# Optimization experiments

Hardware: AMD Instinct MI355X
Metric: run time of the kernel (lower is better)

Reference implementation:

```python
import jax, jax.numpy as jnp
import numpy as np

B, N, NODE_DIM = 32, 512, 2
D, H, L, FF = 512, 8, 3, 2048
DK = D // H  # key/val dim per head = 64
EPS = 1e-5


def batch_norm(h, gamma, beta):
    # BatchNorm1d in training mode over flattened (batch*graph) dim, biased var
    flat = h.reshape(-1, h.shape[-1])
    mu = flat.mean(axis=0)
    var = flat.var(axis=0)
    out = (flat - mu) * jax.lax.rsqrt(var + EPS) * gamma + beta
    return out.reshape(h.shape)


def mha(h, Wq, Wk, Wv, Wo):
    # h: [B,N,D]; Wq/Wk/Wv: [H,D,DK]; Wo: [H,DK,D]
    Q = jnp.einsum('bnd,hdk->hbnk', h, Wq)
    K = jnp.einsum('bnd,hdk->hbnk', h, Wk)
    V = jnp.einsum('bnd,hdk->hbnk', h, Wv)
    scores = jnp.einsum('hbqk,hbnk->hbqn', Q, K) / jnp.sqrt(jnp.float32(DK))
    attn = jax.nn.softmax(scores, axis=-1)
    heads = jnp.einsum('hbqn,hbnk->hbqk', attn, V)
    return jnp.einsum('hbqk,hkd->bqd', heads, Wo)


def setup_inputs() -> dict:
    key = jax.random.key(0)
    ks = jax.random.split(key, 16)
    u = lambda k, shape, fan: jax.random.uniform(k, shape, jnp.float32, -1.0, 1.0) / np.sqrt(fan)
    return {
        'x': jax.random.normal(ks[0], (B, N, NODE_DIM), jnp.float32),
        'We': u(ks[1], (D, NODE_DIM), NODE_DIM),
        'be': u(ks[2], (D,), NODE_DIM),
        'Wq': u(ks[3], (L, H, D, DK), DK),
        'Wk': u(ks[4], (L, H, D, DK), DK),
        'Wv': u(ks[5], (L, H, D, DK), DK),
        'Wo': u(ks[6], (L, H, DK, D), D),
        'g1': jnp.ones((L, D), jnp.float32),
        'b1': jnp.zeros((L, D), jnp.float32),
        'W1': u(ks[7], (L, FF, D), D),
        'bb1': u(ks[8], (L, FF), D),
        'W2': u(ks[9], (L, D, FF), FF),
        'bb2': u(ks[10], (L, D), FF),
        'g2': jnp.ones((L, D), jnp.float32),
        'b2': jnp.zeros((L, D), jnp.float32),
    }


def reference(x, We, be, Wq, Wk, Wv, Wo, g1, b1, W1, bb1, W2, bb2, g2, b2):
    # init embed: Linear(node_dim -> D)
    h = jnp.einsum('bnc,dc->bnd', x, We) + be
    for i in range(L):
        h = batch_norm(h + mha(h, Wq[i], Wk[i], Wv[i], Wo[i]), g1[i], b1[i])
        ff = jax.nn.relu(jnp.einsum('bnd,fd->bnf', h, W1[i]) + bb1[i])
        ff = jnp.einsum('bnf,df->bnd', ff, W2[i]) + bb2[i]
        h = batch_norm(h + ff, g2[i], b2[i])
    return h, h.mean(axis=1)
```

## Files before the change

### kernel.cpp

```cpp
#include <hip/hip_runtime.h>
#include <hip/hip_bf16.h>

#define Bx 32
#define Nx 512
#define Dx 512
#define Hx 8
#define DKx 64
#define FFx 2048
#define TOK (Bx * Nx)
#define EPSx 1e-5f

typedef float  f32x4  __attribute__((ext_vector_type(4)));
typedef _Float16 hfrag8 __attribute__((ext_vector_type(8)));
typedef _Float16 h4     __attribute__((ext_vector_type(4)));
typedef _Float16 h2     __attribute__((ext_vector_type(2)));

struct hf2 { _Float16 hi, lo; };
__device__ __forceinline__ hf2 split2h(float v) {
    _Float16 h = (_Float16)v;
    hf2 r; r.hi = h; r.lo = (_Float16)(v - (float)h);
    return r;
}

__device__ __forceinline__ void gl16(const void* g, void* l) {
    __builtin_amdgcn_global_load_lds(
        (const __attribute__((address_space(1))) unsigned int*)g,
        (__attribute__((address_space(3))) unsigned int*)l, 16, 0, 0);
}

__device__ __forceinline__ int swzoff(int row, int q) {
    int p = row >> 1;
    int sl = ((row & 1) << 2) | q;
    int s = sl ^ (p & 7);
    return p * 128 + s * 16;
}

__device__ __forceinline__ float ldsel(const void* p32, const void* p16, size_t i, int f32) {
    return f32 ? ((const float*)p32)[i]
               : __bfloat162float(((const __hip_bfloat16*)p16)[i]);
}

__global__ void detect_kernel(const void* __restrict__ x, int* __restrict__ flag)
{
    if (threadIdx.x == 0 && blockIdx.x == 0) {
        const unsigned short* u = (const unsigned short*)x;
        int hits = 0;
        for (int i = 0; i < 256; ++i) {
            int e = (u[i] >> 7) & 0xFF;
            if (e >= 0x86) ++hits;
        }
        *flag = (hits > 8) ? 1 : 0;
    }
}

__global__ __launch_bounds__(256) void cvt_kernel(
    const void* __restrict__ W, _Float16* __restrict__ o, const int* __restrict__ dtp)
{
    const int f32 = *dtp;
    size_t idx = (size_t)blockIdx.x * 256 + threadIdx.x;
    o[idx] = (_Float16)ldsel(W, W, idx, f32);
}

__global__ __launch_bounds__(256) void transpose_cvt_kernel(
    const void* __restrict__ W, _Float16* __restrict__ o,
    int R, int C, const int* __restrict__ dtp)
{
    const int f32 = *dtp;
    __shared__ float tile[64][65];
    const size_t mbase = (size_t)blockIdx.z * R * C;
    const int c0 = blockIdx.x * 64, r0 = blockIdx.y * 64;
    const int tc = threadIdx.x & 63, tg = threadIdx.x >> 6;
    #pragma unroll
    for (int i = 0; i < 16; ++i) {
        int r = tg * 16 + i;
        tile[r][tc] = ldsel(W, W, mbase + (size_t)(r0 + r) * C + c0 + tc, f32);
    }
    __syncthreads();
    #pragma unroll
    for (int i = 0; i < 16; ++i) {
        int cc = tg * 16 + i;
        o[mbase + (size_t)(c0 + cc) * R + r0 + tc] = (_Float16)tile[tc][cc];
    }
}

__global__ __launch_bounds__(256) void embed_kernel(
    const void* __restrict__ x, const void* __restrict__ We,
    const void* __restrict__ be, _Float16* __restrict__ hh, _Float16* __restrict__ hl,
    const int* __restrict__ dtp)
{
    const int f32 = *dtp;
    size_t idx = (size_t)blockIdx.x * 256 + threadIdx.x;
    int d = idx & (Dx - 1);
    size_t t = idx >> 9;
    float v = ldsel(x, x, t * 2, f32)     * ldsel(We, We, d * 2, f32) +
              ldsel(x, x, t * 2 + 1, f32) * ldsel(We, We, d * 2 + 1, f32) +
              ldsel(be, be, d, f32);
    hf2 s = split2h(v);
    hh[idx] = s.hi; hl[idx] = s.lo;
}

template <int EPI, int OHF, int STATS>
__global__ __launch_bounds__(256, 3) void gemm3(
    const _Float16* __restrict__ Ahg, const _Float16* __restrict__ Bg,
    const void* __restrict__ bias32, const void* __restrict__ bias16,
    const _Float16* __restrict__ residH, const _Float16* __restrict__ residL,
    void* __restrict__ outp, float* __restrict__ part,
    int M, int N, int K, const int* __restrict__ dtp)
{
    const int f32 = *dtp;
    __shared__ __align__(16) unsigned char lds[3][2 * 8192];

    const int tid = threadIdx.x;
    const int gx = gridDim.x;
    const int nwg = gx * gridDim.y;
    int flat = blockIdx.y * gx + blockIdx.x;
    flat = (flat & 7) * (nwg >> 3) + (flat >> 3);
    const int bm = (flat / gx) * 128;
    const int bn = (flat % gx) * 128;

    const int lane = tid & 63, wv = tid >> 6;
    const int quad = lane >> 4, lrow = lane & 15;
    const int wm = (wv & 1) * 64, wn = (wv >> 1) * 64;

    f32x4 acc[4][4] = {};

    const int s2 = (lane & 7) ^ (lane >> 3);
    const int rl = 2 * (lane >> 3) + (s2 >> 2);
    const int cl = (s2 & 3) * 8;

    const bool doStage = (wv < 2);
    const _Float16* wsrc = (wv == 0) ? Ahg : Bg;
    const int wrb = (wv == 0) ? bm : bn;

    auto stage = [&](int buf, int k0) {
        if (doStage) {
            const _Float16* s = wsrc + (size_t)(wrb + rl) * K + k0 + cl;
            #pragma unroll
            for (int ch = 0; ch < 8; ++ch)
                gl16(s + (size_t)(ch * 16) * K, &lds[buf][wv * 8192 + ch * 1024]);
        }
    };

    int offA[4], offB[4];
    #pragma unroll
    for (int mt = 0; mt < 4; ++mt) offA[mt] = swzoff(wm + mt * 16 + lrow, quad);
    #pragma unroll
    for (int nt = 0; nt < 4; ++nt) offB[nt] = 8192 + swzoff(wn + nt * 16 + lrow, quad);

    const int NT = K >> 5;
    stage(0, 0);
    stage(1, 32);

    for (int i = 0; i < NT; ++i) {
        if (i + 1 < NT) asm volatile("s_waitcnt vmcnt(8)" ::: "memory");
        else            asm volatile("s_waitcnt vmcnt(0)" ::: "memory");
        __builtin_amdgcn_sched_barrier(0);
        __builtin_amdgcn_s_barrier();
        __builtin_amdgcn_sched_barrier(0);

        if (i + 2 < NT) stage((i + 2) % 3, (i + 2) << 5);

        const unsigned char* bp = lds[i % 3];
        hfrag8 ah[4];
        #pragma unroll
        for (int mt = 0; mt < 4; ++mt)
            ah[mt] = *(const hfrag8*)(bp + offA[mt]);
        #pragma unroll
        for (int nt = 0; nt < 4; ++nt) {
            hfrag8 b = *(const hfrag8*)(bp + offB[nt]);
            #pragma unroll
            for (int mt = 0; mt < 4; ++mt)
                acc[mt][nt] = __builtin_amdgcn_mfma_f32_16x16x32_f16(ah[mt], b, acc[mt][nt], 0, 0, 0);
        }

        __builtin_amdgcn_sched_barrier(0);
        asm volatile("s_waitcnt lgkmcnt(0)" ::: "memory");
        __builtin_amdgcn_sched_barrier(0);
    }

    #pragma unroll
    for (int nt = 0; nt < 4; ++nt) {
        const int n = bn + wn + nt * 16 + lrow;
        float cs = 0.f, cq = 0.f;
        #pragma unroll
        for (int mt = 0; mt < 4; ++mt)
            #pragma unroll
            for (int reg = 0; reg < 4; ++reg) {
                int m = bm + wm + mt * 16 + quad * 4 + reg;
                float v = acc[mt][nt][reg];
                if constexpr (EPI == 1) { v += ldsel(bias32, bias16, n, f32); v = fmaxf(v, 0.f); }
                if constexpr (EPI == 2) {
                    if (bias32) v += ldsel(bias32, bias16, n, f32);
                    size_t ridx = (size_t)m * N + n;
                    v += (float)residH[ridx] + (float)residL[ridx];
                }
                size_t oidx = (size_t)m * N + n;
                if constexpr (OHF == 1) ((_Float16*)outp)[oidx] = (_Float16)v;
                else if constexpr (OHF == 2) {
                    hf2 s = split2h(v);
                    h2 pk; pk[0] = s.hi; pk[1] = s.lo;
                    ((h2*)outp)[oidx] = pk;
                }
                else ((float*)outp)[oidx] = v;
                if constexpr (STATS) { cs += v; cq += v * v; }
            }
        if constexpr (STATS) {
            cs += __shfl_xor(cs, 16); cs += __shfl_xor(cs, 32);
            cq += __shfl_xor(cq, 16); cq += __shfl_xor(cq, 32);
            if (quad == 0) {
                float* pb = part + (size_t)(bm >> 7) * 1024;
                atomicAdd(&pb[n], cs);
                atomicAdd(&pb[512 + n], cq);
            }
        }
    }
}

__global__ __launch_bounds__(256, 3) void qkv_mfma(
    const _Float16* __restrict__ Ahg,
    const _Float16* __restrict__ QT, const _Float16* __restrict__ KT,
    const _Float16* __restrict__ VT,
    _Float16* __restrict__ Qhg, _Float16* __restrict__ Qlg,
    _Float16* __restrict__ Khg, _Float16* __restrict__ Vo, int M, int K)
{
    __shared__ __align__(16) unsigned char lds[3][2 * 8192];

    const int tid = threadIdx.x;
    const int gx = gridDim.x;
    const int nwg = gx * gridDim.y;
    int flat = blockIdx.y * gx + blockIdx.x;
    flat = (flat & 7) * (nwg >> 3) + (flat >> 3);
    const int bm = (flat / gx) * 128;
    const int bn = (flat % gx) * 128;

    const int sel = bn >> 9;
    const int nloc = bn & 511;
    const _Float16* Bg = ((sel == 0) ? QT : (sel == 1) ? KT : VT) + (size_t)nloc * K;

    const int lane = tid & 63, wv = tid >> 6;
    const int quad = lane >> 4, lrow = lane & 15;
    const int wm = (wv & 1) * 64, wn = (wv >> 1) * 64;

    f32x4 acc[4][4] = {};

    const int s2 = (lane & 7) ^ (lane >> 3);
    const int rl = 2 * (lane >> 3) + (s2 >> 2);
    const int cl = (s2 & 3) * 8;

    const bool doStage = (wv < 2);
    const _Float16* wsrc = (wv == 0) ? Ahg : Bg;
    const int wrb = (wv == 0) ? bm : 0;

    auto stage = [&](int buf, int k0) {
        if (doStage) {
            const _Float16* s = wsrc + (size_t)(wrb + rl) * K + k0 + cl;
            #pragma unroll
            for (int ch = 0; ch < 8; ++ch)
                gl16(s + (size_t)(ch * 16) * K, &lds[buf][wv * 8192 + ch * 1024]);
        }
    };

    int offA[4], offB[4];
    #pragma unroll
    for (int mt = 0; mt < 4; ++mt) offA[mt] = swzoff(wm + mt * 16 + lrow, quad);
    #pragma unroll
    for (int nt = 0; nt < 4; ++nt) offB[nt] = 8192 + swzoff(wn + nt * 16 + lrow, quad);

    const int NT = K >> 5;
    stage(0, 0);
    stage(1, 32);

    for (int i = 0; i < NT; ++i) {
        if (i + 1 < NT) asm volatile("s_waitcnt vmcnt(8)" ::: "memory");
        else            asm volatile("s_waitcnt vmcnt(0)" ::: "memory");
        __builtin_amdgcn_sched_barrier(0);
        __builtin_amdgcn_s_barrier();
        __builtin_amdgcn_sched_barrier(0);

        if (i + 2 < NT) stage((i + 2) % 3, (i + 2) << 5);

        const unsigned char* bp = lds[i % 3];
        hfrag8 ah[4];
        #pragma unroll
        for (int mt = 0; mt < 4; ++mt)
            ah[mt] = *(const hfrag8*)(bp + offA[mt]);
        #pragma unroll
        for (int nt = 0; nt < 4; ++nt) {
            hfrag8 b = *(const hfrag8*)(bp + offB[nt]);
            #pragma unroll
            for (int mt = 0; mt < 4; ++mt)
                acc[mt][nt] = __builtin_amdgcn_mfma_f32_16x16x32_f16(ah[mt], b, acc[mt][nt], 0, 0, 0);
        }

        __builtin_amdgcn_sched_barrier(0);
        asm volatile("s_waitcnt lgkmcnt(0)" ::: "memory");
        __builtin_amdgcn_sched_barrier(0);
    }

    const int nb = M >> 9;
    #pragma unroll
    for (int mt = 0; mt < 4; ++mt)
        #pragma unroll
        for (int nt = 0; nt < 4; ++nt) {
            const int ncol = nloc + wn + nt * 16 + lrow;
            const int head = ncol >> 6, dk = ncol & 63;
            const int m0 = bm + wm + mt * 16 + quad * 4;
            const int b_ = m0 >> 9, q = m0 & 511;
            if (sel == 2) {
                h4 v;
                #pragma unroll
                for (int reg = 0; reg < 4; ++reg) v[reg] = (_Float16)acc[mt][nt][reg];
                *(h4*)&Vo[(((size_t)head * nb + b_) * DKx + dk) * Nx + q] = v;
            } else if (sel == 1) {
                #pragma unroll
                for (int reg = 0; reg < 4; ++reg) {
                    size_t oidx = (((size_t)head * nb + b_) * Nx + (q + reg)) * DKx + dk;
                    Khg[oidx] = (_Float16)acc[mt][nt][reg];
                }
            } else {
                #pragma unroll
                for (int reg = 0; reg < 4; ++reg) {
                    hf2 s = split2h(acc[mt][nt][reg]);
                    size_t oidx = (((size_t)head * nb + b_) * Nx + (q + reg)) * DKx + dk;
                    Qhg[oidx] = s.hi;
                    Qlg[oidx] = s.lo;
                }
            }
        }
}

__global__ __launch_bounds__(256, 4) void attn_kernel(
    const _Float16* __restrict__ Qhg, const _Float16* __restrict__ Qlg,
    const _Float16* __restrict__ Khg, const _Float16* __restrict__ Vtg,
    _Float16* __restrict__ heads)
{
    __shared__ __align__(16) _Float16  Kh[64][72];
    __shared__ __align__(16) _Float16  Vt[64][72];
    __shared__ __align__(16) _Float16  Sp[64][72];
    __shared__ float ml[64], ll[64], al[64];

    const int tid = threadIdx.x;
    const int q0 = blockIdx.x * 64;
    const int hb = blockIdx.y;
    const size_t base = (size_t)hb * (Nx * DKx);
    const int lane = tid & 63, wv = tid >> 6;
    const int quad = lane >> 4, lrow = lane & 15;
    const int wm = (wv & 1) * 32, wn = (wv >> 1) * 32;
    const int sr = tid >> 2, sc = (tid & 3) * 16;

    {
        size_t off = base + (size_t)(q0 + sr) * DKx + sc;
        *(hfrag8*)&Kh[sr][sc]     = *(const hfrag8*)(Qhg + off);
        *(hfrag8*)&Kh[sr][sc + 8] = *(const hfrag8*)(Qhg + off + 8);
        *(hfrag8*)&Sp[sr][sc]     = *(const hfrag8*)(Qlg + off);
        *(hfrag8*)&Sp[sr][sc + 8] = *(const hfrag8*)(Qlg + off + 8);
    }
    if (tid < 64) { ml[tid] = -INFINITY; ll[tid] = 0.f; }
    __syncthreads();

    hfrag8 qh[2][2], qlo[2][2];
    #pragma unroll
    for (int mt = 0; mt < 2; ++mt)
        #pragma unroll
        for (int ks = 0; ks < 2; ++ks) {
            qh[mt][ks]  = *(const hfrag8*)&Kh[wm + mt * 16 + lrow][ks * 32 + quad * 8];
            qlo[mt][ks] = *(const hfrag8*)&Sp[wm + mt * 16 + lrow][ks * 32 + quad * 8];
        }
    __syncthreads();

    hfrag8 pkh[2], pv[2];
    auto loadKV = [&](int n0) {
        size_t off = base + (size_t)(n0 + sr) * DKx + sc;
        pkh[0] = *(const hfrag8*)(Khg + off);
        pkh[1] = *(const hfrag8*)(Khg + off + 8);
        const _Float16* vp = Vtg + base + (size_t)sr * Nx + n0 + sc;
        pv[0] = *(const hfrag8*)vp;
        pv[1] = *(const hfrag8*)(vp + 8);
    };
    auto storeKV = [&]() {
        *(hfrag8*)&Kh[sr][sc]     = pkh[0];
        *(hfrag8*)&Kh[sr][sc + 8] = pkh[1];
        *(hfrag8*)&Vt[sr][sc]     = pv[0];
        *(hfrag8*)&Vt[sr][sc + 8] = pv[1];
    };

    f32x4 accO[2][2] = {};

    loadKV(0); storeKV();
    __syncthreads();

    for (int n0 = 0; n0 < Nx; n0 += 64) {
        const bool more = (n0 + 64 < Nx);
        if (more) loadKV(n0 + 64);

        f32x4 accS[2][2] = {};
        __builtin_amdgcn_s_setprio(1);
        #pragma unroll
        for (int ks = 0; ks < 2; ++ks) {
            hfrag8 bh[2];
            #pragma unroll
            for (int nt = 0; nt < 2; ++nt)
                bh[nt] = *(const hfrag8*)&Kh[wn + nt * 16 + lrow][ks * 32 + quad * 8];
            #pragma unroll
            for (int mt = 0; mt < 2; ++mt)
                #pragma unroll
                for (int nt = 0; nt < 2; ++nt) {
                    accS[mt][nt] = __builtin_amdgcn_mfma_f32_16x16x32_f16(qh[mt][ks],  bh[nt], accS[mt][nt], 0, 0, 0);
                    accS[mt][nt] = __builtin_amdgcn_mfma_f32_16x16x32_f16(qlo[mt][ks], bh[nt], accS[mt][nt], 0, 0, 0);
                }
        }
        __builtin_amdgcn_s_setprio(0);
        #pragma unroll
        for (int mt = 0; mt < 2; ++mt)
            #pragma unroll
            for (int nt = 0; nt < 2; ++nt)
                #pragma unroll
                for (int reg = 0; reg < 4; ++reg)
                    Sp[wm + mt * 16 + quad * 4 + reg][wn + nt * 16 + lrow] =
                        (_Float16)(accS[mt][nt][reg] * 0.125f);
        __syncthreads();

        {
            hfrag8 s0 = *(const hfrag8*)&Sp[sr][sc];
            hfrag8 s1 = *(const hfrag8*)&Sp[sr][sc + 8];
            float rmax = -INFINITY;
            #pragma unroll
            for (int j = 0; j < 8; ++j) {
                rmax = fmaxf(rmax, (float)s0[j]);
                rmax = fmaxf(rmax, (float)s1[j]);
            }
            rmax = fmaxf(rmax, __shfl_xor(rmax, 1));
            rmax = fmaxf(rmax, __shfl_xor(rmax, 2));
            float mold = ml[sr];
            float mnew = fmaxf(mold, rmax);
            float sum = 0.f;
            hfrag8 p0, p1;
            #pragma unroll
            for (int j = 0; j < 8; ++j) {
                float pa = __expf((float)s0[j] - mnew);
                float pb = __expf((float)s1[j] - mnew);
                sum += pa + pb;
                p0[j] = (_Float16)pa;
                p1[j] = (_Float16)pb;
            }
            sum += __shfl_xor(sum, 1);
            sum += __shfl_xor(sum, 2);
            *(hfrag8*)&Sp[sr][sc]     = p0;
            *(hfrag8*)&Sp[sr][sc + 8] = p1;
            if ((tid & 3) == 0) {
                float alpha = __expf(mold - mnew);
                ml[sr] = mnew;
                ll[sr] = ll[sr] * alpha + sum;
                al[sr] = alpha;
            }
        }
        __syncthreads();

        #pragma unroll
        for (int mt = 0; mt < 2; ++mt) {
            float a0 = al[wm + mt * 16 + quad * 4 + 0];
            float a1 = al[wm + mt * 16 + quad * 4 + 1];
            float a2 = al[wm + mt * 16 + quad * 4 + 2];
            float a3 = al[wm + mt * 16 + quad * 4 + 3];
            #pragma unroll
            for (int nt = 0; nt < 2; ++nt) {
                accO[mt][nt][0] *= a0; accO[mt][nt][1] *= a1;
                accO[mt][nt][2] *= a2; accO[mt][nt][3] *= a3;
            }
        }
        __builtin_amdgcn_s_setprio(1);
        #pragma unroll
        for (int ks = 0; ks < 2; ++ks) {
            hfrag8 ap[2], bv[2];
            #pragma unroll
            for (int mt = 0; mt < 2; ++mt)
                ap[mt] = *(const hfrag8*)&Sp[wm + mt * 16 + lrow][ks * 32 + quad * 8];
            #pragma unroll
            for (int nt = 0; nt < 2; ++nt)
                bv[nt] = *(const hfrag8*)&Vt[wn + nt * 16 + lrow][ks * 32 + quad * 8];
            #pragma unroll
            for (int mt = 0; mt < 2; ++mt)
                #pragma unroll
                for (int nt = 0; nt < 2; ++nt)
                    accO[mt][nt] = __builtin_amdgcn_mfma_f32_16x16x32_f16(ap[mt], bv[nt], accO[mt][nt], 0, 0, 0);
        }
        __builtin_amdgcn_s_setprio(0);

        if (more) {
            __syncthreads();
            storeKV();
            __syncthreads();
        }
    }

    const int h_ = hb >> 5, b_ = hb & 31;
    #pragma unroll
    for (int mt = 0; mt < 2; ++mt)
        #pragma unroll
        for (int reg = 0; reg < 4; ++reg) {
            int qrow = wm + mt * 16 + quad * 4 + reg;
            float invl = 1.f / ll[qrow];
            size_t tok = (size_t)b_ * Nx + (q0 + qrow);
            #pragma unroll
            for (int nt = 0; nt < 2; ++nt) {
                int dk = wn + nt * 16 + lrow;
                heads[tok * Dx + h_ * DKx + dk] = (_Float16)(accO[mt][nt][reg] * invl);
            }
        }
}

__global__ __launch_bounds__(256) void bn_final(
    const float* __restrict__ part, float* __restrict__ stats)
{
    int c = blockIdx.x * 256 + threadIdx.x;
    float s = 0.f;
    for (int rt = 0; rt < 128; ++rt) s += part[(size_t)rt * 1024 + c];
    stats[c] = s;
}

__global__ __launch_bounds__(256) void bn_norm(
    const h2* __restrict__ tpk, const float* __restrict__ stats,
    const void* __restrict__ g32, const void* __restrict__ g16,
    const void* __restrict__ b32, const void* __restrict__ b16,
    _Float16* __restrict__ hh, _Float16* __restrict__ hl,
    float* __restrict__ out32, const int* __restrict__ dtp)
{
    const int f32 = *dtp;
    size_t idx = (size_t)blockIdx.x * 256 + threadIdx.x;
    int c = idx & (Dx - 1);
    const float invM = 1.f / (float)TOK;
    float mu = stats[c] * invM;
    float var = stats[Dx + c] * invM - mu * mu;
    h2 tv = tpk[idx];
    float t = (float)tv[0] + (float)tv[1];
    float v = (t - mu) * rsqrtf(var + EPSx) * ldsel(g32, g16, c, f32) + ldsel(b32, b16, c, f32);
    hf2 s = split2h(v);
    hh[idx] = s.hi; hl[idx] = s.lo;
    if (out32) out32[idx] = v;
}

__global__ __launch_bounds__(256) void out_mean_part(
    const _Float16* __restrict__ hh, const _Float16* __restrict__ hl, float* __restrict__ part)
{
    int b = blockIdx.x;
    int g = blockIdx.y;
    int d = threadIdx.x;
    float s0 = 0.f, s1 = 0.f;
    for (int n = g * 64; n < g * 64 + 64; ++n) {
        size_t idx = ((size_t)b * Nx + n) * Dx;
        s0 += (float)hh[idx + d]       + (float)hl[idx + d];
        s1 += (float)hh[idx + d + 256] + (float)hl[idx + d + 256];
    }
    part[((size_t)b * 8 + g) * Dx + d]       = s0;
    part[((size_t)b * 8 + g) * Dx + d + 256] = s1;
}

__global__ __launch_bounds__(256) void out_mean_final(
    const float* __restrict__ part, float* __restrict__ out2)
{
    size_t o = (size_t)blockIdx.x * 256 + threadIdx.x;
    int b = (int)(o >> 9), d = (int)(o & 511);
    float s = 0.f;
    #pragma unroll
    for (int g = 0; g < 8; ++g) s += part[((size_t)b * 8 + g) * Dx + d];
    out2[o] = s * (1.f / (float)Nx);
}

extern "C" void kernel_launch(void* const* d_in, const int* in_sizes, int n_in,
                              void* d_out, int out_size, void* d_ws, size_t ws_size,
                              hipStream_t stream)
{
    const void* x   = d_in[0];
    const void* We  = d_in[1];
    const void* be  = d_in[2];
    const void* Wq  = d_in[3];
    const void* Wk  = d_in[4];
    const void* Wv  = d_in[5];
    const void* Wo  = d_in[6];
    const void* g1  = d_in[7];
    const void* b1  = d_in[8];
    const void* W1  = d_in[9];
    const void* bb1 = d_in[10];
    const void* W2  = d_in[11];
    const void* bb2 = d_in[12];
    const void* g2  = d_in[13];
    const void* b2  = d_in[14];

    const size_t szHD = (size_t)TOK * Dx;
    const size_t QKN  = (size_t)Hx * Bx * Nx * DKx;
    const size_t szQT = (size_t)3 * Hx * DKx * Dx;
    const size_t szW1 = (size_t)3 * FFx * Dx;
    const size_t szWqkvL = (size_t)Hx * Dx * DKx;

    h2* tpk        = (h2*)d_ws;
    float* stats   = (float*)(tpk + szHD);
    int*   dtp     = (int*)(stats + 2 * Dx);
    _Float16* hh   = (_Float16*)(stats + 2 * Dx + 64);
    _Float16* hl   = hh + szHD;
    _Float16* region = hl + szHD;

    _Float16* heads = region;
    _Float16* Qhg   = heads + szHD;
    _Float16* Qlg   = Qhg + QKN;
    _Float16* Khg   = Qlg + QKN;
    _Float16* Vtg   = Khg + QKN;
    _Float16* ffbuf = region;

    _Float16* WqT = Vtg + QKN;
    _Float16* WkT = WqT + szQT;
    _Float16* WvT = WkT + szQT;
    _Float16* WoT = WvT + szQT;
    _Float16* W1c = WoT + szQT;
    _Float16* W2c = W1c + szW1;
    float*    part = (float*)(W2c + szW1);

    auto p32 = [](const void* p, size_t e) { return (const void*)((const float*)p + e); };
    auto p16 = [](const void* p, size_t e) { return (const void*)((const __hip_bfloat16*)p + e); };

    detect_kernel<<<1, 64, 0, stream>>>(x, dtp);

    transpose_cvt_kernel<<<dim3(1, 8, 24), 256, 0, stream>>>(Wq, WqT, Dx, DKx, dtp);
    transpose_cvt_kernel<<<dim3(1, 8, 24), 256, 0, stream>>>(Wk, WkT, Dx, DKx, dtp);
    transpose_cvt_kernel<<<dim3(1, 8, 24), 256, 0, stream>>>(Wv, WvT, Dx, DKx, dtp);
    transpose_cvt_kernel<<<dim3(8, 8, 3), 256, 0, stream>>>(Wo, WoT, Dx, Dx, dtp);
    cvt_kernel<<<szW1 / 256, 256, 0, stream>>>(W1, W1c, dtp);
    cvt_kernel<<<szW1 / 256, 256, 0, stream>>>(W2, W2c, dtp);

    embed_kernel<<<TOK * Dx / 256, 256, 0, stream>>>(x, We, be, hh, hl, dtp);

    const dim3 gQKV(12, TOK / 128);
    const dim3 gWo(Dx / 128, TOK / 128);
    const dim3 gAttn(Nx / 64, Hx * Bx);
    const dim3 gFF1(FFx / 128, TOK / 128);
    const dim3 gFF2(Dx / 128, TOK / 128);
    const size_t partBytes = 128 * 1024 * sizeof(float);
    for (int l = 0; l < 3; ++l) {
        const size_t eQ = (size_t)l * szWqkvL;
        const size_t e1 = (size_t)l * FFx * Dx;
        const size_t eD = (size_t)l * Dx, eF = (size_t)l * FFx;
        const bool last = (l == 2);

        qkv_mfma<<<gQKV, 256, 0, stream>>>(
            hh, WqT + eQ, WkT + eQ, WvT + eQ,
            Qhg, Qlg, Khg, Vtg, TOK, Dx);
        attn_kernel<<<gAttn, 256, 0, stream>>>(Qhg, Qlg, Khg, Vtg, heads);

        hipMemsetAsync(part, 0, partBytes, stream);
        gemm3<2, 2, 1><<<gWo, 256, 0, stream>>>(
            heads, WoT + eQ,
            nullptr, nullptr, hh, hl, tpk, part, TOK, Dx, Dx, dtp);
        bn_final<<<4, 256, 0, stream>>>(part, stats);
        bn_norm<<<TOK * Dx / 256, 256, 0, stream>>>(
            tpk, stats, p32(g1, eD), p16(g1, eD), p32(b1, eD), p16(b1, eD),
            hh, hl, nullptr, dtp);

        gemm3<1, 1, 0><<<gFF1, 256, 0, stream>>>(
            hh, W1c + e1,
            p32(bb1, eF), p16(bb1, eF), nullptr, nullptr, ffbuf, nullptr,
            TOK, FFx, Dx, dtp);
        hipMemsetAsync(part, 0, partBytes, stream);
        gemm3<2, 2, 1><<<gFF2, 256, 0, stream>>>(
            ffbuf, W2c + e1,
            p32(bb2, eD), p16(bb2, eD), hh, hl, tpk, part, TOK, Dx, FFx, dtp);
        bn_final<<<4, 256, 0, stream>>>(part, stats);
        bn_norm<<<TOK * Dx / 256, 256, 0, stream>>>(
            tpk, stats, p32(g2, eD), p16(g2, eD), p32(b2, eD), p16(b2, eD),
            hh, hl, last ? (float*)d_out : nullptr, dtp);
    }

    out_mean_part<<<dim3(Bx, 8), 256, 0, stream>>>(hh, hl, part);
    out_mean_final<<<Bx * Dx / 256, 256, 0, stream>>>(part, (float*)d_out + (size_t)TOK * Dx);
}
```

Measured before the change: 1.200 ms.

## Widen GEMM output tiles to 128x256 with three staging waves

Both the generic GEMM and the fused QKV GEMM move from 128x128 to 128x256 output tiles. Each wave now holds a 64x128 accumulator, and a third wave stages the second half of the B tile into a larger LDS buffer. The aim is better operand reuse per LDS load and fewer A-tile reloads from global memory. In exchange, register pressure roughly doubles, occupancy bounds drop from 3 to 2 workgroups, and the grids shrink by half. The batch-norm partial buffer is enlarged and indexed by 64-row blocks, and bn_final now sums 256 partial rows.

```diff
diff --git a/kernel.cpp b/kernel.cpp
--- a/kernel.cpp
+++ b/kernel.cpp
@@ -100,7 +100,7 @@
 }
 
 template <int EPI, int OHF, int STATS>
-__global__ __launch_bounds__(256, 3) void gemm3(
+__global__ __launch_bounds__(256, 2) void gemm3(
     const _Float16* __restrict__ Ahg, const _Float16* __restrict__ Bg,
     const void* __restrict__ bias32, const void* __restrict__ bias16,
     const _Float16* __restrict__ residH, const _Float16* __restrict__ residL,
@@ -108,7 +108,7 @@
     int M, int N, int K, const int* __restrict__ dtp)
 {
     const int f32 = *dtp;
-    __shared__ __align__(16) unsigned char lds[3][2 * 8192];
+    __shared__ __align__(16) unsigned char lds[3][24576];
 
     const int tid = threadIdx.x;
     const int gx = gridDim.x;
@@ -116,40 +116,44 @@
     int flat = blockIdx.y * gx + blockIdx.x;
     flat = (flat & 7) * (nwg >> 3) + (flat >> 3);
     const int bm = (flat / gx) * 128;
-    const int bn = (flat % gx) * 128;
+    const int bn = (flat % gx) * 256;
 
     const int lane = tid & 63, wv = tid >> 6;
     const int quad = lane >> 4, lrow = lane & 15;
-    const int wm = (wv & 1) * 64, wn = (wv >> 1) * 64;
-
-    f32x4 acc[4][4] = {};
+    const int wm = (wv & 1) * 64, wn = (wv >> 1) * 128;
+
+    f32x4 acc[4][8] = {};
 
     const int s2 = (lane & 7) ^ (lane >> 3);
     const int rl = 2 * (lane >> 3) + (s2 >> 2);
     const int cl = (s2 & 3) * 8;
 
-    const bool doStage = (wv < 2);
-    const _Float16* wsrc = (wv == 0) ? Ahg : Bg;
-    const int wrb = (wv == 0) ? bm : bn;
-
-    auto stage = [&](int buf, int k0) {
-        if (doStage) {
+    const _Float16* wsrc = nullptr;
+    int wrb = 0, wbase = 0;
+    if (wv == 0)      { wsrc = Ahg; wrb = bm;       wbase = 0; }
+    else if (wv == 1) { wsrc = Bg;  wrb = bn;       wbase = 8192; }
+    else if (wv == 2) { wsrc = Bg;  wrb = bn + 128; wbase = 16384; }
+
+    auto stage = [&](int step) {
+        if (wsrc) {
+            const int buf = step % 3;
+            const int k0 = step << 5;
             const _Float16* s = wsrc + (size_t)(wrb + rl) * K + k0 + cl;
             #pragma unroll
             for (int ch = 0; ch < 8; ++ch)
-                gl16(s + (size_t)(ch * 16) * K, &lds[buf][wv * 8192 + ch * 1024]);
+                gl16(s + (size_t)(ch * 16) * K, &lds[buf][wbase + ch * 1024]);
         }
     };
 
-    int offA[4], offB[4];
+    int offA[4], offB[8];
     #pragma unroll
     for (int mt = 0; mt < 4; ++mt) offA[mt] = swzoff(wm + mt * 16 + lrow, quad);
     #pragma unroll
-    for (int nt = 0; nt < 4; ++nt) offB[nt] = 8192 + swzoff(wn + nt * 16 + lrow, quad);
+    for (int nt = 0; nt < 8; ++nt) offB[nt] = 8192 + swzoff(wn + nt * 16 + lrow, quad);
 
     const int NT = K >> 5;
-    stage(0, 0);
-    stage(1, 32);
+    stage(0);
+    stage(1);
 
     for (int i = 0; i < NT; ++i) {
         if (i + 1 < NT) asm volatile("s_waitcnt vmcnt(8)" ::: "memory");
@@ -158,7 +162,7 @@
         __builtin_amdgcn_s_barrier();
         __builtin_amdgcn_sched_barrier(0);
 
-        if (i + 2 < NT) stage((i + 2) % 3, (i + 2) << 5);
+        if (i + 2 < NT) stage(i + 2);
 
         const unsigned char* bp = lds[i % 3];
         hfrag8 ah[4];
@@ -166,7 +170,7 @@
         for (int mt = 0; mt < 4; ++mt)
             ah[mt] = *(const hfrag8*)(bp + offA[mt]);
         #pragma unroll
-        for (int nt = 0; nt < 4; ++nt) {
+        for (int nt = 0; nt < 8; ++nt) {
             hfrag8 b = *(const hfrag8*)(bp + offB[nt]);
             #pragma unroll
             for (int mt = 0; mt < 4; ++mt)
@@ -179,7 +183,7 @@
     }
 
     #pragma unroll
-    for (int nt = 0; nt < 4; ++nt) {
+    for (int nt = 0; nt < 8; ++nt) {
         const int n = bn + wn + nt * 16 + lrow;
         float cs = 0.f, cq = 0.f;
         #pragma unroll
@@ -208,7 +212,7 @@
             cs += __shfl_xor(cs, 16); cs += __shfl_xor(cs, 32);
             cq += __shfl_xor(cq, 16); cq += __shfl_xor(cq, 32);
             if (quad == 0) {
-                float* pb = part + (size_t)(bm >> 7) * 1024;
+                float* pb = part + (size_t)(bm >> 6) * 1024;
                 atomicAdd(&pb[n], cs);
                 atomicAdd(&pb[512 + n], cq);
             }
@@ -216,14 +220,14 @@
     }
 }
 
-__global__ __launch_bounds__(256, 3) void qkv_mfma(
+__global__ __launch_bounds__(256, 2) void qkv_mfma(
     const _Float16* __restrict__ Ahg,
     const _Float16* __restrict__ QT, const _Float16* __restrict__ KT,
     const _Float16* __restrict__ VT,
     _Float16* __restrict__ Qhg, _Float16* __restrict__ Qlg,
     _Float16* __restrict__ Khg, _Float16* __restrict__ Vo, int M, int K)
 {
-    __shared__ __align__(16) unsigned char lds[3][2 * 8192];
+    __shared__ __align__(16) unsigned char lds[3][24576];
 
     const int tid = threadIdx.x;
     const int gx = gridDim.x;
@@ -231,7 +235,7 @@
     int flat = blockIdx.y * gx + blockIdx.x;
     flat = (flat & 7) * (nwg >> 3) + (flat >> 3);
     const int bm = (flat / gx) * 128;
-    const int bn = (flat % gx) * 128;
+    const int bn = (flat % gx) * 256;
 
     const int sel = bn >> 9;
     const int nloc = bn & 511;
@@ -239,36 +243,40 @@
 
     const int lane = tid & 63, wv = tid >> 6;
     const int quad = lane >> 4, lrow = lane & 15;
-    const int wm = (wv & 1) * 64, wn = (wv >> 1) * 64;
-
-    f32x4 acc[4][4] = {};
+    const int wm = (wv & 1) * 64, wn = (wv >> 1) * 128;
+
+    f32x4 acc[4][8] = {};
 
     const int s2 = (lane & 7) ^ (lane >> 3);
     const int rl = 2 * (lane >> 3) + (s2 >> 2);
     const int cl = (s2 & 3) * 8;
 
-    const bool doStage = (wv < 2);
-    const _Float16* wsrc = (wv == 0) ? Ahg : Bg;
-    const int wrb = (wv == 0) ? bm : 0;
-
-    auto stage = [&](int buf, int k0) {
-        if (doStage) {
+    const _Float16* wsrc = nullptr;
+    int wrb = 0, wbase = 0;
+    if (wv == 0)      { wsrc = Ahg; wrb = bm;  wbase = 0; }
+    else if (wv == 1) { wsrc = Bg;  wrb = 0;   wbase = 8192; }
+    else if (wv == 2) { wsrc = Bg;  wrb = 128; wbase = 16384; }
+
+    auto stage = [&](int step) {
+        if (wsrc) {
+            const int buf = step % 3;
+            const int k0 = step << 5;
             const _Float16* s = wsrc + (size_t)(wrb + rl) * K + k0 + cl;
             #pragma unroll
             for (int ch = 0; ch < 8; ++ch)
-                gl16(s + (size_t)(ch * 16) * K, &lds[buf][wv * 8192 + ch * 1024]);
+                gl16(s + (size_t)(ch * 16) * K, &lds[buf][wbase + ch * 1024]);
         }
     };
 
-    int offA[4], offB[4];
+    int offA[4], offB[8];
     #pragma unroll
     for (int mt = 0; mt < 4; ++mt) offA[mt] = swzoff(wm + mt * 16 + lrow, quad);
     #pragma unroll
-    for (int nt = 0; nt < 4; ++nt) offB[nt] = 8192 + swzoff(wn + nt * 16 + lrow, quad);
+    for (int nt = 0; nt < 8; ++nt) offB[nt] = 8192 + swzoff(wn + nt * 16 + lrow, quad);
 
     const int NT = K >> 5;
-    stage(0, 0);
-    stage(1, 32);
+    stage(0);
+    stage(1);
 
     for (int i = 0; i < NT; ++i) {
         if (i + 1 < NT) asm volatile("s_waitcnt vmcnt(8)" ::: "memory");
@@ -277,7 +285,7 @@
         __builtin_amdgcn_s_barrier();
         __builtin_amdgcn_sched_barrier(0);
 
-        if (i + 2 < NT) stage((i + 2) % 3, (i + 2) << 5);
+        if (i + 2 < NT) stage(i + 2);
 
         const unsigned char* bp = lds[i % 3];
         hfrag8 ah[4];
@@ -285,7 +293,7 @@
         for (int mt = 0; mt < 4; ++mt)
             ah[mt] = *(const hfrag8*)(bp + offA[mt]);
         #pragma unroll
-        for (int nt = 0; nt < 4; ++nt) {
+        for (int nt = 0; nt < 8; ++nt) {
             hfrag8 b = *(const hfrag8*)(bp + offB[nt]);
             #pragma unroll
             for (int mt = 0; mt < 4; ++mt)
@@ -301,7 +309,7 @@
     #pragma unroll
     for (int mt = 0; mt < 4; ++mt)
         #pragma unroll
-        for (int nt = 0; nt < 4; ++nt) {
+        for (int nt = 0; nt < 8; ++nt) {
             const int ncol = nloc + wn + nt * 16 + lrow;
             const int head = ncol >> 6, dk = ncol & 63;
             const int m0 = bm + wm + mt * 16 + quad * 4;
@@ -514,7 +522,7 @@
 {
     int c = blockIdx.x * 256 + threadIdx.x;
     float s = 0.f;
-    for (int rt = 0; rt < 128; ++rt) s += part[(size_t)rt * 1024 + c];
+    for (int rt = 0; rt < 256; ++rt) s += part[(size_t)rt * 1024 + c];
     stats[c] = s;
 }
 
@@ -628,12 +636,12 @@
 
     embed_kernel<<<TOK * Dx / 256, 256, 0, stream>>>(x, We, be, hh, hl, dtp);
 
-    const dim3 gQKV(12, TOK / 128);
-    const dim3 gWo(Dx / 128, TOK / 128);
+    const dim3 gQKV(6, TOK / 128);
+    const dim3 gWo(Dx / 256, TOK / 128);
     const dim3 gAttn(Nx / 64, Hx * Bx);
-    const dim3 gFF1(FFx / 128, TOK / 128);
-    const dim3 gFF2(Dx / 128, TOK / 128);
-    const size_t partBytes = 128 * 1024 * sizeof(float);
+    const dim3 gFF1(FFx / 256, TOK / 128);
+    const dim3 gFF2(Dx / 256, TOK / 128);
+    const size_t partBytes = 256 * 1024 * sizeof(float);
     for (int l = 0; l < 3; ++l) {
         const size_t eQ = (size_t)l * szWqkvL;
         const size_t e1 = (size_t)l * FFx * Dx;
```

After: 1.268 ms. 5.7% more time.
